# Optimization experiments

Hardware: AMD Instinct MI355X
Metric: run time of the kernel (lower is better)

## Reference

```python
import jax, jax.numpy as jnp
import numpy as np

B, S = 2, 2048          # 2 prompt sequences of 2048 tokens (packed: T = B*S)
H, KV, D, G = 32, 8, 128, 128   # heads, kv heads, head_dim, quant group size
THETA = 1e6


def _dequant(w_int, scales, g=G):
    # w_int: [O, I] int4 values in [-8, 7]; scales: [O, I//g] per-group fp scales
    return w_int.astype(jnp.float32) * jnp.repeat(scales, g, axis=1)


def _rope_neox(x, pos):
    # x: [B, S, h, D]; pos: [B, S]; neox style rotates (first half, second half)
    half = D // 2
    inv_freq = 1.0 / (THETA ** (jnp.arange(half, dtype=jnp.float32) / half))
    ang = pos[:, :, None] * inv_freq[None, None, :]          # [B, S, half]
    cos = jnp.cos(ang)[:, :, None, :]
    sin = jnp.sin(ang)[:, :, None, :]
    x1, x2 = x[..., :half], x[..., half:]
    return jnp.concatenate([x1 * cos - x2 * sin, x2 * cos + x1 * sin], axis=-1)


def setup_inputs() -> dict:
    key = jax.random.key(0)
    k1, k2, k3, k4, k5, k6 = jax.random.split(key, 6)
    T, HID = B * S, H * D
    q_hidden = jax.random.randint(k1, (T, HID), -127, 128, dtype=jnp.int32)  # int8 acts
    q_scale = jax.random.uniform(k2, (T,), dtype=jnp.float32) * 0.01 + 1e-4  # per-token scale
    q_sum = jnp.sum(q_hidden, axis=-1).astype(jnp.float32)                   # per-token int8 sum
    OUT_QKV = (H + 2 * KV) * D
    w_qkv = jax.random.randint(k3, (OUT_QKV, HID), -8, 8, dtype=jnp.int32)   # int4 weights
    s_qkv = jax.random.uniform(k4, (OUT_QKV, HID // G), dtype=jnp.float32) * 0.01 + 1e-4
    w_o = jax.random.randint(k5, (HID, HID), -8, 8, dtype=jnp.int32)
    s_o = jax.random.uniform(k6, (HID, HID // G), dtype=jnp.float32) * 0.01 + 1e-4
    return {"q_hidden": q_hidden, "q_scale": q_scale, "q_sum": q_sum,
            "w_qkv": w_qkv, "s_qkv": s_qkv, "w_o": w_o, "s_o": s_o}


def reference(q_hidden, q_scale, q_sum, w_qkv, s_qkv, w_o, s_o):
    T = q_hidden.shape[0]
    # W4A8 qkv_proj with dynamic per-token input scale (symmetric int4 -> sum unused)
    x = q_hidden.astype(jnp.float32) * q_scale[:, None]          # dequant activations
    qkv = x @ _dequant(w_qkv, s_qkv).T                            # [T, (H+2KV)*D]
    q_sz, kv_sz = H * D, KV * D
    q = qkv[:, :q_sz].reshape(B, S, H, D)
    k = qkv[:, q_sz:q_sz + kv_sz].reshape(B, S, KV, D)
    v = qkv[:, q_sz + kv_sz:].reshape(B, S, KV, D)
    # fused bias(none)+RoPE (neox, full head_dim)
    pos = jnp.broadcast_to(jnp.arange(S, dtype=jnp.float32), (B, S))
    q = _rope_neox(q, pos)
    k = _rope_neox(k, pos)
    # varlen causal flash attention (GQA: 4 q-heads per kv head)
    qg = q.reshape(B, S, KV, H // KV, D)
    scores = jnp.einsum('bsghd,btgd->bghst', qg, k) * (D ** -0.5)
    causal = jnp.tril(jnp.ones((S, S), dtype=bool))
    scores = jnp.where(causal[None, None, None], scores, -jnp.inf)
    p = jax.nn.softmax(scores, axis=-1)
    attn = jnp.einsum('bghst,btgd->bsghd', p, v).reshape(T, H * D)
    # invoke_quant_fuse_sum: per-token symmetric int8 requant of attn output
    amax = jnp.maximum(jnp.max(jnp.abs(attn), axis=-1, keepdims=True), 1e-6)
    a_scale = amax / 127.0
    attn_q = jnp.clip(jnp.round(attn / a_scale), -127.0, 127.0)
    # W4A8 o_proj
    out = (attn_q * a_scale) @ _dequant(w_o, s_o).T               # [T, H*D]
    return out
```

## Files before the change

kernel.cpp:

```cpp
#include <hip/hip_runtime.h>
#include <math.h>

#define B_ 2
#define S_ 2048
#define H_ 32
#define KV_ 8
#define D_ 128
#define T_ 4096
#define HID_ 4096
#define OQKV_ 6144

typedef __attribute__((ext_vector_type(4))) float f32x4;
typedef __attribute__((ext_vector_type(4))) int i32x4;
typedef __attribute__((ext_vector_type(8))) __bf16 bf16x8;
typedef __attribute__((ext_vector_type(8))) unsigned short u16x8;
typedef unsigned short u16;
typedef signed char s8;

__device__ __forceinline__ u16 f2b(float f) {
  unsigned x = __float_as_uint(f);
  return (u16)((x + 0x7FFFu + ((x >> 16) & 1u)) >> 16);
}
__device__ __forceinline__ float b2f(u16 u) {
  return __uint_as_float(((unsigned)u) << 16);
}

__device__ __forceinline__ void async16(const void* g, void* l) {
  __builtin_amdgcn_global_load_lds((__attribute__((address_space(1))) void*)g,
                                   (__attribute__((address_space(3))) void*)l,
                                   16, 0, 0);
}

__device__ __forceinline__ bf16x8 ld8(const u16* p) { return *(const bf16x8*)p; }

__device__ __forceinline__ f32x4 mfma16x16(bf16x8 a, bf16x8 b, f32x4 c) {
  return __builtin_amdgcn_mfma_f32_16x16x32_bf16(a, b, c, 0, 0, 0);
}

__device__ __forceinline__ bf16x8 ones8() {
  union { u16x8 u; bf16x8 b; } c;
  c.u = u16x8{0x3F80, 0x3F80, 0x3F80, 0x3F80, 0x3F80, 0x3F80, 0x3F80, 0x3F80};
  return c.b;
}

__global__ __launch_bounds__(256) void pack_i8(const int* __restrict__ w,
                                               s8* __restrict__ out) {
  size_t base = ((size_t)blockIdx.x * 256 + threadIdx.x) * 4;
  int4 v = *(const int4*)(w + base);
  unsigned r = (unsigned)(v.x & 255) | ((unsigned)(v.y & 255) << 8) |
               ((unsigned)(v.z & 255) << 16) | ((unsigned)v.w << 24);
  *(unsigned*)(out + base) = r;
}

__global__ __launch_bounds__(256) void rope_kernel(u16* __restrict__ qkv) {
  int idx = blockIdx.x * 256 + threadIdx.x;
  int t = idx / 2560;
  int r = idx - t * 2560;
  int head = r >> 6;
  int d = r & 63;
  int col = (head < 32) ? (head * 128 + d) : (4096 + (head - 32) * 128 + d);
  size_t base = (size_t)t * 6144 + col;
  float x1 = b2f(qkv[base]);
  float x2 = b2f(qkv[base + 64]);
  float e = (float)d * 0.015625f;
  float freq = exp2f(e * -19.931568569324174f);
  float ang = (float)(t & 2047) * freq;
  float sn, cs;
  sincosf(ang, &sn, &cs);
  qkv[base] = f2b(x1 * cs - x2 * sn);
  qkv[base + 64] = f2b(x2 * cs + x1 * sn);
}

__global__ __launch_bounds__(256) void vt_transpose(const u16* __restrict__ qkv,
                                                    u16* __restrict__ vt) {
  __shared__ u16 tile[64][65];
  const int s0 = blockIdx.x * 64, d0 = blockIdx.y * 64;
  const int bk = blockIdx.z, b = bk >> 3, kv = bk & 7;
  const int tid = threadIdx.x;
  const int rr = tid >> 3, cc = tid & 7;
#pragma unroll
  for (int it = 0; it < 2; it++) {
    int r = it * 32 + rr;
    u16x8 v = *(const u16x8*)(qkv + (size_t)(b * 2048 + s0 + r) * 6144 + 5120 +
                              kv * 128 + d0 + cc * 8);
#pragma unroll
    for (int k = 0; k < 8; k++) tile[r][cc * 8 + k] = v[k];
  }
  __syncthreads();
#pragma unroll
  for (int it = 0; it < 2; it++) {
    int d = it * 32 + rr;
    u16x8 o;
#pragma unroll
    for (int k = 0; k < 8; k++) o[k] = tile[cc * 8 + k][d];
    *(u16x8*)(vt + (size_t)(bk * 128 + d0 + d) * 2048 + s0 + cc * 8) = o;
  }
}

__device__ __forceinline__ void store_out(float* p, float v) { *p = v; }
__device__ __forceinline__ void store_out(u16* p, float v) { *p = f2b(v); }

template <typename OutT>
__global__ __launch_bounds__(256) void gemm_i8(const s8* __restrict__ A,
                                               const s8* __restrict__ Bw,
                                               const float* __restrict__ sB,
                                               const float* __restrict__ rowscale,
                                               OutT* __restrict__ C,
                                               int M, int N, int K) {
  __shared__ __align__(16) s8 As[128 * 64];
  __shared__ __align__(16) s8 Bs[128 * 64];
  __shared__ float Ss[128][33];
  const int tid = threadIdx.x;
  const int lane = tid & 63;
  const int wv = tid >> 6;
  const int wm = wv >> 1, wn = wv & 1;
  const int m0 = blockIdx.y * 128, n0 = blockIdx.x * 128;
  const int g = lane >> 4, c15 = lane & 15;
  const int KG = K >> 7;

  for (int i = tid; i < 128 * 32; i += 256)
    Ss[i >> 5][i & 31] = sB[(size_t)n0 * 32 + i];

  f32x4 acc[4][4] = {};

  const int c0 = 2 * wv, c1 = c0 + 1;
  const int srow = lane >> 2;
  const int pch = lane & 3;
  const int scol = (((pch - (srow >> 1)) & 3)) * 16;
  const s8* Ag0 = A + (size_t)(m0 + c0 * 16 + srow) * K + scol;
  const s8* Ag1 = A + (size_t)(m0 + c1 * 16 + srow) * K + scol;
  const s8* Bg0 = Bw + (size_t)(n0 + c0 * 16 + srow) * K + scol;
  const s8* Bg1 = Bw + (size_t)(n0 + c1 * 16 + srow) * K + scol;
  s8* Al0 = As + c0 * 1024 + lane * 16;
  s8* Al1 = As + c1 * 1024 + lane * 16;
  s8* Bl0 = Bs + c0 * 1024 + lane * 16;
  s8* Bl1 = Bs + c1 * 1024 + lane * 16;

  for (int grp = 0; grp < KG; grp++) {
    i32x4 iacc[4][4];
#pragma unroll
    for (int sub = 0; sub < 2; sub++) {
      const int kb = grp * 128 + sub * 64;
      __syncthreads();
      async16(Ag0 + kb, Al0);
      async16(Ag1 + kb, Al1);
      async16(Bg0 + kb, Bl0);
      async16(Bg1 + kb, Bl1);
      __syncthreads();
      i32x4 af[4], bf[4];
#pragma unroll
      for (int i = 0; i < 4; i++) {
        af[i] = *(const i32x4*)(As + (wm * 64 + i * 16 + c15) * 64 +
                                ((g + (c15 >> 1)) & 3) * 16);
        bf[i] = *(const i32x4*)(Bs + (wn * 64 + i * 16 + c15) * 64 +
                                ((g + (c15 >> 1)) & 3) * 16);
      }
#pragma unroll
      for (int i = 0; i < 4; i++)
#pragma unroll
        for (int j = 0; j < 4; j++)
          iacc[i][j] = __builtin_amdgcn_mfma_i32_16x16x64_i8(
              af[i], bf[j], sub ? iacc[i][j] : (i32x4){0, 0, 0, 0}, 0, 0, 0);
    }
#pragma unroll
    for (int j = 0; j < 4; j++) {
      const float sc = Ss[wn * 64 + j * 16 + c15][grp];
#pragma unroll
      for (int i = 0; i < 4; i++)
#pragma unroll
        for (int r = 0; r < 4; r++)
          acc[i][j][r] += sc * (float)iacc[i][j][r];
    }
  }

#pragma unroll
  for (int i = 0; i < 4; i++) {
#pragma unroll
    for (int r = 0; r < 4; r++) {
      int m = m0 + wm * 64 + i * 16 + g * 4 + r;
      float scm = rowscale[m];
#pragma unroll
      for (int j = 0; j < 4; j++) {
        int n = n0 + wn * 64 + j * 16 + c15;
        store_out(C + (size_t)m * N + n, acc[i][j][r] * scm);
      }
    }
  }
}

struct AttnState {
  f32x4 acc[2][9];
  float mrun[2][4];
};

template <bool FULL>
__device__ __forceinline__ void attn_step(
    int j0, int q0, const u16* kbase, const u16* vbase, u16* pw0, u16* pw1,
    const bf16x8 qf[2][4], AttnState& st, int g, int c15, const bf16x8 vones) {
  const int qmax = q0 + 31;
  f32x4 sc[2][4];
#pragma unroll
  for (int nt = 0; nt < 4; nt++) {
    if (FULL || (j0 + nt * 16 <= qmax)) {
      bf16x8 kf[4];
      const u16* kp = kbase + (size_t)(j0 + nt * 16) * 6144;
#pragma unroll
      for (int c = 0; c < 4; c++) kf[c] = ld8(kp + c * 32);
      f32x4 s0 = {0.f, 0.f, 0.f, 0.f}, s1 = {0.f, 0.f, 0.f, 0.f};
#pragma unroll
      for (int c = 0; c < 4; c++) {
        s0 = mfma16x16(qf[0][c], kf[c], s0);
        s1 = mfma16x16(qf[1][c], kf[c], s1);
      }
      if (FULL) {
#pragma unroll
        for (int r = 0; r < 4; r++) {
          sc[0][nt][r] = s0[r] * 0.08838834764831845f;
          sc[1][nt][r] = s1[r] * 0.08838834764831845f;
        }
      } else {
        const int key = j0 + nt * 16 + c15;
#pragma unroll
        for (int r = 0; r < 4; r++) {
          sc[0][nt][r] =
              (key <= q0 + g * 4 + r) ? s0[r] * 0.08838834764831845f : -INFINITY;
          sc[1][nt][r] =
              (key <= q0 + 16 + g * 4 + r) ? s1[r] * 0.08838834764831845f : -INFINITY;
        }
      }
    }
  }
#pragma unroll
  for (int m = 0; m < 2; m++) {
    u16* pw = m ? pw1 : pw0;
    float alpha[4];
#pragma unroll
    for (int r = 0; r < 4; r++) {
      float rm = -INFINITY;
#pragma unroll
      for (int nt = 0; nt < 4; nt++)
        if (FULL || (j0 + nt * 16 <= qmax)) rm = fmaxf(rm, sc[m][nt][r]);
      rm = fmaxf(rm, __shfl_xor(rm, 1));
      rm = fmaxf(rm, __shfl_xor(rm, 2));
      rm = fmaxf(rm, __shfl_xor(rm, 4));
      rm = fmaxf(rm, __shfl_xor(rm, 8));
      float mnew = fmaxf(st.mrun[m][r], rm);
      alpha[r] = __expf(st.mrun[m][r] - mnew);
      st.mrun[m][r] = mnew;
#pragma unroll
      for (int nt = 0; nt < 4; nt++) {
        float pv = (FULL || (j0 + nt * 16 <= qmax))
                       ? __expf(sc[m][nt][r] - mnew) : 0.0f;
        pw[(g * 4 + r) * 72 + nt * 16 + c15] = f2b(pv);
      }
    }
#pragma unroll
    for (int dt = 0; dt < 9; dt++)
#pragma unroll
      for (int r = 0; r < 4; r++) st.acc[m][dt][r] *= alpha[r];
  }
#pragma unroll
  for (int kc = 0; kc < 2; kc++) {
    bf16x8 pf0 = ld8(pw0 + c15 * 72 + kc * 32 + g * 8);
    bf16x8 pf1 = ld8(pw1 + c15 * 72 + kc * 32 + g * 8);
#pragma unroll
    for (int dt = 0; dt < 8; dt++) {
      bf16x8 vf = ld8(vbase + (size_t)(dt * 16) * 2048 + j0 + kc * 32);
      st.acc[0][dt] = mfma16x16(pf0, vf, st.acc[0][dt]);
      st.acc[1][dt] = mfma16x16(pf1, vf, st.acc[1][dt]);
    }
    st.acc[0][8] = mfma16x16(pf0, vones, st.acc[0][8]);
    st.acc[1][8] = mfma16x16(pf1, vones, st.acc[1][8]);
  }
}

__global__ __launch_bounds__(256, 2) void attn_kernel(const u16* __restrict__ qkvb,
                                                      const u16* __restrict__ vtb,
                                                      float* __restrict__ out) {
  __shared__ __align__(16) u16 Ps[4][2][16 * 72];
  const int tid = threadIdx.x, lane = tid & 63, wv = tid >> 6;
  const int g = lane >> 4, c15 = lane & 15;
  const int a = blockIdx.x * 4 + wv;
  const int h = blockIdx.y, b = blockIdx.z, kvh = h >> 2;
  const bf16x8 vones = ones8();
  const u16* kbase =
      qkvb + (size_t)(b * 2048 + c15) * 6144 + 4096 + kvh * 128 + g * 8;
  const u16* vbase = vtb + (size_t)((b * 8 + kvh) * 128 + c15) * 2048 + g * 8;
  u16* pw0 = &Ps[wv][0][0];
  u16* pw1 = &Ps[wv][1][0];

  for (int half = 0; half < 2; half++) {
    const int qt = half ? (63 - a) : a;
    const int q0 = qt * 32;
    bf16x8 qf[2][4];
#pragma unroll
    for (int m = 0; m < 2; m++) {
      const u16* qp =
          qkvb + (size_t)(b * 2048 + q0 + m * 16 + c15) * 6144 + h * 128 + g * 8;
#pragma unroll
      for (int c = 0; c < 4; c++) qf[m][c] = ld8(qp + c * 32);
    }
    AttnState st;
#pragma unroll
    for (int m = 0; m < 2; m++)
#pragma unroll
      for (int dt = 0; dt < 9; dt++) st.acc[m][dt] = f32x4{0.f, 0.f, 0.f, 0.f};
#pragma unroll
    for (int m = 0; m < 2; m++)
#pragma unroll
      for (int r = 0; r < 4; r++) st.mrun[m][r] = -INFINITY;

    const int nfull = qt >> 1;
    for (int jt = 0; jt < nfull; jt++)
      attn_step<true>(jt * 64, q0, kbase, vbase, pw0, pw1, qf, st, g, c15, vones);
    attn_step<false>(nfull * 64, q0, kbase, vbase, pw0, pw1, qf, st, g, c15, vones);

#pragma unroll
    for (int m = 0; m < 2; m++)
#pragma unroll
      for (int r = 0; r < 4; r++) {
        const int row = q0 + m * 16 + g * 4 + r;
        float inv = 1.0f / st.acc[m][8][r];
        float* op = out + (size_t)(b * 2048 + row) * 4096 + h * 128;
#pragma unroll
        for (int dt = 0; dt < 8; dt++) op[dt * 16 + c15] = st.acc[m][dt][r] * inv;
      }
  }
}

__global__ __launch_bounds__(256) void quant_kernel(const float* __restrict__ attn,
                                                    s8* __restrict__ aq,
                                                    float* __restrict__ ascale) {
  const int t = blockIdx.x, tid = threadIdx.x;
  const float* row = attn + (size_t)t * 4096;
  f32x4 v[4];
  float am = 0.f;
#pragma unroll
  for (int i = 0; i < 4; i++) {
    v[i] = *(const f32x4*)(row + tid * 16 + i * 4);
#pragma unroll
    for (int r = 0; r < 4; r++) am = fmaxf(am, fabsf(v[i][r]));
  }
#pragma unroll
  for (int m = 1; m <= 32; m <<= 1) am = fmaxf(am, __shfl_xor(am, m));
  __shared__ float red[4];
  if ((tid & 63) == 0) red[tid >> 6] = am;
  __syncthreads();
  am = fmaxf(fmaxf(red[0], red[1]), fmaxf(red[2], red[3]));
  float asc = fmaxf(am, 1e-6f) / 127.0f;
  if (tid == 0) ascale[t] = asc;
  int w[4];
#pragma unroll
  for (int i = 0; i < 4; i++) {
    int bytes[4];
#pragma unroll
    for (int r = 0; r < 4; r++) {
      float q = rintf(v[i][r] / asc);
      q = fminf(127.0f, fmaxf(-127.0f, q));
      bytes[r] = ((int)q) & 255;
    }
    w[i] = bytes[0] | (bytes[1] << 8) | (bytes[2] << 16) | (bytes[3] << 24);
  }
  *(int4*)(aq + (size_t)t * 4096 + tid * 16) = int4{w[0], w[1], w[2], w[3]};
}

extern "C" void kernel_launch(void* const* d_in, const int* in_sizes, int n_in,
                              void* d_out, int out_size, void* d_ws, size_t ws_size,
                              hipStream_t stream) {
  const int* q_hidden = (const int*)d_in[0];
  const float* q_scale = (const float*)d_in[1];
  const int* w_qkv = (const int*)d_in[3];
  const float* s_qkv = (const float*)d_in[4];
  const int* w_o = (const int*)d_in[5];
  const float* s_o = (const float*)d_in[6];
  float* out = (float*)d_out;

  char* ws = (char*)d_ws;
  const size_t MB = 1024 * 1024;
  s8* WB = (s8*)(ws);
  u16* QKVB = (u16*)(ws + 48 * MB);
  u16* VTB = (u16*)(ws);
  s8* ATTNQ = (s8*)(ws + 8 * MB);
  float* ASC = (float*)(ws + 25 * MB);
  s8* WOB = (s8*)(ws + 48 * MB);
  s8* XB = (s8*)d_out;

  pack_i8<<<16384, 256, 0, stream>>>(q_hidden, XB);
  pack_i8<<<24576, 256, 0, stream>>>(w_qkv, WB);
  gemm_i8<u16><<<dim3(48, 32), 256, 0, stream>>>(XB, WB, s_qkv, q_scale, QKVB,
                                                 T_, OQKV_, HID_);
  rope_kernel<<<40960, 256, 0, stream>>>(QKVB);
  vt_transpose<<<dim3(32, 2, 16), 256, 0, stream>>>(QKVB, VTB);
  attn_kernel<<<dim3(8, 32, 2), 256, 0, stream>>>(QKVB, VTB, out);
  quant_kernel<<<4096, 256, 0, stream>>>(out, ATTNQ, ASC);
  pack_i8<<<16384, 256, 0, stream>>>(w_o, WOB);
  gemm_i8<float><<<dim3(32, 32), 256, 0, stream>>>(ATTNQ, WOB, s_o, ASC, out,
                                                   T_, HID_, HID_);
}
```

Baseline: 802.4 us.

## Split attention KV loop across wave pairs with shared-memory softmax merge

Each query tile is now handled by two waves, each covering half of the causal KV range. The partial accumulators and running maxima are merged through shared memory with a rescaled flash-decoding style combine. The grid doubles and launch bounds request 4 blocks per CU, aiming for more parallelism and occupancy in the attention kernel. The cost is extra block-wide syncs, shared-memory traffic, and possible register pressure or spills under the tighter launch bound.

Result: slower. 997.3 us (+24.3%).

```diff
diff --git a/kernel.cpp b/kernel.cpp
--- a/kernel.cpp
+++ b/kernel.cpp
@@ -274,13 +274,15 @@
   }
 }
 
-__global__ __launch_bounds__(256, 2) void attn_kernel(const u16* __restrict__ qkvb,
+__global__ __launch_bounds__(256, 4) void attn_kernel(const u16* __restrict__ qkvb,
                                                       const u16* __restrict__ vtb,
                                                       float* __restrict__ out) {
   __shared__ __align__(16) u16 Ps[4][2][16 * 72];
+  __shared__ __align__(16) float Sc[2][10][64][4];
   const int tid = threadIdx.x, lane = tid & 63, wv = tid >> 6;
   const int g = lane >> 4, c15 = lane & 15;
-  const int a = blockIdx.x * 4 + wv;
+  const int pair = wv & 1, sub = wv >> 1;
+  const int a = blockIdx.x * 2 + pair;
   const int h = blockIdx.y, b = blockIdx.z, kvh = h >> 2;
   const bf16x8 vones = ones8();
   const u16* kbase =
@@ -311,20 +313,59 @@
       for (int r = 0; r < 4; r++) st.mrun[m][r] = -INFINITY;
 
     const int nfull = qt >> 1;
-    for (int jt = 0; jt < nfull; jt++)
-      attn_step<true>(jt * 64, q0, kbase, vbase, pw0, pw1, qf, st, g, c15, vones);
-    attn_step<false>(nfull * 64, q0, kbase, vbase, pw0, pw1, qf, st, g, c15, vones);
-
-#pragma unroll
-    for (int m = 0; m < 2; m++)
-#pragma unroll
-      for (int r = 0; r < 4; r++) {
-        const int row = q0 + m * 16 + g * 4 + r;
-        float inv = 1.0f / st.acc[m][8][r];
-        float* op = out + (size_t)(b * 2048 + row) * 4096 + h * 128;
-#pragma unroll
-        for (int dt = 0; dt < 8; dt++) op[dt * 16 + c15] = st.acc[m][dt][r] * inv;
-      }
+    const int ns = nfull + 1;
+    const int ns0 = ns >> 1;
+    if (sub == 0) {
+      for (int jt = 0; jt < ns0; jt++)
+        attn_step<true>(jt * 64, q0, kbase, vbase, pw0, pw1, qf, st, g, c15, vones);
+    } else {
+      for (int jt = ns0; jt < nfull; jt++)
+        attn_step<true>(jt * 64, q0, kbase, vbase, pw0, pw1, qf, st, g, c15, vones);
+      attn_step<false>(nfull * 64, q0, kbase, vbase, pw0, pw1, qf, st, g, c15, vones);
+    }
+
+#pragma unroll
+    for (int mt = 0; mt < 2; mt++) {
+      __syncthreads();
+      if (sub == 1) {
+#pragma unroll
+        for (int dt = 0; dt < 9; dt++)
+          *(f32x4*)&Sc[pair][dt][lane][0] = st.acc[mt][dt];
+        *(f32x4*)&Sc[pair][9][lane][0] =
+            f32x4{st.mrun[mt][0], st.mrun[mt][1], st.mrun[mt][2], st.mrun[mt][3]};
+      }
+      __syncthreads();
+      if (sub == 0) {
+        f32x4 m2 = *(const f32x4*)&Sc[pair][9][lane][0];
+        float a0[4], a1[4];
+#pragma unroll
+        for (int r = 0; r < 4; r++) {
+          float mn = fmaxf(st.mrun[mt][r], m2[r]);
+          a0[r] = __expf(st.mrun[mt][r] - mn);
+          a1[r] = __expf(m2[r] - mn);
+        }
+#pragma unroll
+        for (int dt = 0; dt < 9; dt++) {
+          f32x4 o = *(const f32x4*)&Sc[pair][dt][lane][0];
+#pragma unroll
+          for (int r = 0; r < 4; r++)
+            st.acc[mt][dt][r] = st.acc[mt][dt][r] * a0[r] + o[r] * a1[r];
+        }
+      }
+    }
+
+    if (sub == 0) {
+#pragma unroll
+      for (int m = 0; m < 2; m++)
+#pragma unroll
+        for (int r = 0; r < 4; r++) {
+          const int row = q0 + m * 16 + g * 4 + r;
+          float inv = 1.0f / st.acc[m][8][r];
+          float* op = out + (size_t)(b * 2048 + row) * 4096 + h * 128;
+#pragma unroll
+          for (int dt = 0; dt < 8; dt++) op[dt * 16 + c15] = st.acc[m][dt][r] * inv;
+        }
+    }
   }
 }
 
@@ -391,7 +432,7 @@
                                                  T_, OQKV_, HID_);
   rope_kernel<<<40960, 256, 0, stream>>>(QKVB);
   vt_transpose<<<dim3(32, 2, 16), 256, 0, stream>>>(QKVB, VTB);
-  attn_kernel<<<dim3(8, 32, 2), 256, 0, stream>>>(QKVB, VTB, out);
+  attn_kernel<<<dim3(16, 32, 2), 256, 0, stream>>>(QKVB, VTB, out);
   quant_kernel<<<4096, 256, 0, stream>>>(out, ATTNQ, ASC);
   pack_i8<<<16384, 256, 0, stream>>>(w_o, WOB);
   gemm_i8<float><<<dim3(32, 32), 256, 0, stream>>>(ATTNQ, WOB, s_o, ASC, out,
```

## Stage K/V tiles in shared memory with async double-buffered loads in attention

Applied to the files above, without the earlier changes.

The attention kernel now assigns each block a 128-row query tile (four warps of 32 rows) and cooperatively stages 64-key K and V tiles into swizzled shared memory with async copies. V is double-buffered so the next tile loads during softmax and PV. This replaces per-warp direct global loads and removes redundant K/V traffic across the warps of a block. The grid is reordered to launch the heaviest causal tiles first. The price is extra LDS use, two barriers per step, and the loss of the earlier pairing of short and long tiles inside each warp for load balance.

Result: faster. 693.9 us (-13.5%).

```diff
diff --git a/kernel.cpp b/kernel.cpp
--- a/kernel.cpp
+++ b/kernel.cpp
@@ -188,24 +188,25 @@
   }
 }
 
+
 struct AttnState {
   f32x4 acc[2][9];
   float mrun[2][4];
 };
 
 template <bool FULL>
-__device__ __forceinline__ void attn_step(
-    int j0, int q0, const u16* kbase, const u16* vbase, u16* pw0, u16* pw1,
-    const bf16x8 qf[2][4], AttnState& st, int g, int c15, const bf16x8 vones) {
-  const int qmax = q0 + 31;
-  f32x4 sc[2][4];
+__device__ __forceinline__ void qk_phase(int j0, int q0w, const u16* Ksp,
+                                         const bf16x8 qf[2][4],
+                                         f32x4 (&sc)[2][4], int g, int c15) {
+  const int qmax = q0w + 31;
 #pragma unroll
   for (int nt = 0; nt < 4; nt++) {
     if (FULL || (j0 + nt * 16 <= qmax)) {
       bf16x8 kf[4];
-      const u16* kp = kbase + (size_t)(j0 + nt * 16) * 6144;
-#pragma unroll
-      for (int c = 0; c < 4; c++) kf[c] = ld8(kp + c * 32);
+#pragma unroll
+      for (int c = 0; c < 4; c++)
+        kf[c] = ld8(Ksp + (nt * 16 + c15) * 128 +
+                    (((g + 4 * c) ^ (c15 & 7)) * 8));
       f32x4 s0 = {0.f, 0.f, 0.f, 0.f}, s1 = {0.f, 0.f, 0.f, 0.f};
 #pragma unroll
       for (int c = 0; c < 4; c++) {
@@ -223,13 +224,21 @@
 #pragma unroll
         for (int r = 0; r < 4; r++) {
           sc[0][nt][r] =
-              (key <= q0 + g * 4 + r) ? s0[r] * 0.08838834764831845f : -INFINITY;
+              (key <= q0w + g * 4 + r) ? s0[r] * 0.08838834764831845f : -INFINITY;
           sc[1][nt][r] =
-              (key <= q0 + 16 + g * 4 + r) ? s1[r] * 0.08838834764831845f : -INFINITY;
+              (key <= q0w + 16 + g * 4 + r) ? s1[r] * 0.08838834764831845f : -INFINITY;
         }
       }
     }
   }
+}
+
+template <bool FULL>
+__device__ __forceinline__ void smax_pv(int j0, int q0w, const u16* Vsp,
+                                        u16* pw0, u16* pw1, f32x4 (&sc)[2][4],
+                                        AttnState& st, int g, int c15,
+                                        const bf16x8 vones) {
+  const int qmax = q0w + 31;
 #pragma unroll
   for (int m = 0; m < 2; m++) {
     u16* pw = m ? pw1 : pw0;
@@ -265,7 +274,8 @@
     bf16x8 pf1 = ld8(pw1 + c15 * 72 + kc * 32 + g * 8);
 #pragma unroll
     for (int dt = 0; dt < 8; dt++) {
-      bf16x8 vf = ld8(vbase + (size_t)(dt * 16) * 2048 + j0 + kc * 32);
+      bf16x8 vf = ld8(Vsp + (dt * 16 + c15) * 64 +
+                      (((g + 4 * kc) ^ (c15 & 7)) * 8));
       st.acc[0][dt] = mfma16x16(pf0, vf, st.acc[0][dt]);
       st.acc[1][dt] = mfma16x16(pf1, vf, st.acc[1][dt]);
     }
@@ -277,55 +287,90 @@
 __global__ __launch_bounds__(256, 2) void attn_kernel(const u16* __restrict__ qkvb,
                                                       const u16* __restrict__ vtb,
                                                       float* __restrict__ out) {
+  __shared__ __align__(16) u16 Ks[64 * 128];
+  __shared__ __align__(16) u16 Vs[2][128 * 64];
   __shared__ __align__(16) u16 Ps[4][2][16 * 72];
   const int tid = threadIdx.x, lane = tid & 63, wv = tid >> 6;
   const int g = lane >> 4, c15 = lane & 15;
-  const int a = blockIdx.x * 4 + wv;
-  const int h = blockIdx.y, b = blockIdx.z, kvh = h >> 2;
+  const int h = blockIdx.x, b = blockIdx.y, qb = 15 - (int)blockIdx.z;
+  const int kvh = h >> 2;
+  const int Q0 = qb * 128;
+  const int q0w = Q0 + wv * 32;
+  const int nsteps = 2 * qb + 2;
   const bf16x8 vones = ones8();
-  const u16* kbase =
-      qkvb + (size_t)(b * 2048 + c15) * 6144 + 4096 + kvh * 128 + g * 8;
-  const u16* vbase = vtb + (size_t)((b * 8 + kvh) * 128 + c15) * 2048 + g * 8;
   u16* pw0 = &Ps[wv][0][0];
   u16* pw1 = &Ps[wv][1][0];
 
-  for (int half = 0; half < 2; half++) {
-    const int qt = half ? (63 - a) : a;
-    const int q0 = qt * 32;
-    bf16x8 qf[2][4];
-#pragma unroll
-    for (int m = 0; m < 2; m++) {
-      const u16* qp =
-          qkvb + (size_t)(b * 2048 + q0 + m * 16 + c15) * 6144 + h * 128 + g * 8;
-#pragma unroll
-      for (int c = 0; c < 4; c++) qf[m][c] = ld8(qp + c * 32);
-    }
-    AttnState st;
-#pragma unroll
-    for (int m = 0; m < 2; m++)
-#pragma unroll
-      for (int dt = 0; dt < 9; dt++) st.acc[m][dt] = f32x4{0.f, 0.f, 0.f, 0.f};
-#pragma unroll
-    for (int m = 0; m < 2; m++)
-#pragma unroll
-      for (int r = 0; r < 4; r++) st.mrun[m][r] = -INFINITY;
-
-    const int nfull = qt >> 1;
-    for (int jt = 0; jt < nfull; jt++)
-      attn_step<true>(jt * 64, q0, kbase, vbase, pw0, pw1, qf, st, g, c15, vones);
-    attn_step<false>(nfull * 64, q0, kbase, vbase, pw0, pw1, qf, st, g, c15, vones);
-
-#pragma unroll
-    for (int m = 0; m < 2; m++)
-#pragma unroll
-      for (int r = 0; r < 4; r++) {
-        const int row = q0 + m * 16 + g * 4 + r;
-        float inv = 1.0f / st.acc[m][8][r];
-        float* op = out + (size_t)(b * 2048 + row) * 4096 + h * 128;
-#pragma unroll
-        for (int dt = 0; dt < 8; dt++) op[dt * 16 + c15] = st.acc[m][dt][r] * inv;
-      }
-  }
+  const int keyl = lane >> 4, kch = lane & 15;
+  const int dll = lane >> 3, vch = lane & 7;
+  const u16* Kg = qkvb + (size_t)(b * 2048) * 6144 + 4096 + kvh * 128;
+  const u16* Vg = vtb + (size_t)((b * 8 + kvh) * 128) * 2048;
+
+  auto stageK = [&](int j0) {
+#pragma unroll
+    for (int i = 0; i < 4; i++) {
+      const int key = wv * 16 + i * 4 + keyl;
+      async16(Kg + (size_t)(j0 + key) * 6144 + ((kch ^ (key & 7)) * 8),
+              (u16*)Ks + (wv * 16 + i * 4) * 128 + lane * 8);
+    }
+  };
+  auto stageV = [&](int j0, int vb) {
+#pragma unroll
+    for (int i = 0; i < 4; i++) {
+      const int d = wv * 32 + i * 8 + dll;
+      async16(Vg + (size_t)d * 2048 + j0 + ((vch ^ (d & 7)) * 8),
+              (u16*)&Vs[vb][0] + (wv * 32 + i * 8) * 64 + lane * 8);
+    }
+  };
+
+  bf16x8 qf[2][4];
+#pragma unroll
+  for (int m = 0; m < 2; m++) {
+    const u16* qp =
+        qkvb + (size_t)(b * 2048 + q0w + m * 16 + c15) * 6144 + h * 128 + g * 8;
+#pragma unroll
+    for (int c = 0; c < 4; c++) qf[m][c] = ld8(qp + c * 32);
+  }
+
+  AttnState st;
+#pragma unroll
+  for (int m = 0; m < 2; m++) {
+#pragma unroll
+    for (int dt = 0; dt < 9; dt++) st.acc[m][dt] = f32x4{0.f, 0.f, 0.f, 0.f};
+#pragma unroll
+    for (int r = 0; r < 4; r++) st.mrun[m][r] = -INFINITY;
+  }
+
+  stageK(0);
+  stageV(0, 0);
+
+  for (int jt = 0; jt < nsteps; ++jt) {
+    const int j0 = jt * 64;
+    __syncthreads();
+    const int mode = (j0 + 64 <= q0w) ? 0 : ((j0 <= q0w + 31) ? 1 : 2);
+    f32x4 sc[2][4];
+    if (mode == 0) qk_phase<true>(j0, q0w, (const u16*)Ks, qf, sc, g, c15);
+    else if (mode == 1) qk_phase<false>(j0, q0w, (const u16*)Ks, qf, sc, g, c15);
+    __syncthreads();
+    if (jt + 1 < nsteps) {
+      stageK(j0 + 64);
+      stageV(j0 + 64, (jt + 1) & 1);
+    }
+    const u16* Vsp = (const u16*)&Vs[jt & 1][0];
+    if (mode == 0) smax_pv<true>(j0, q0w, Vsp, pw0, pw1, sc, st, g, c15, vones);
+    else if (mode == 1) smax_pv<false>(j0, q0w, Vsp, pw0, pw1, sc, st, g, c15, vones);
+  }
+
+#pragma unroll
+  for (int m = 0; m < 2; m++)
+#pragma unroll
+    for (int r = 0; r < 4; r++) {
+      const int row = q0w + m * 16 + g * 4 + r;
+      float inv = 1.0f / st.acc[m][8][r];
+      float* op = out + (size_t)(b * 2048 + row) * 4096 + h * 128;
+#pragma unroll
+      for (int dt = 0; dt < 8; dt++) op[dt * 16 + c15] = st.acc[m][dt][r] * inv;
+    }
 }
 
 __global__ __launch_bounds__(256) void quant_kernel(const float* __restrict__ attn,
@@ -391,7 +436,7 @@
                                                  T_, OQKV_, HID_);
   rope_kernel<<<40960, 256, 0, stream>>>(QKVB);
   vt_transpose<<<dim3(32, 2, 16), 256, 0, stream>>>(QKVB, VTB);
-  attn_kernel<<<dim3(8, 32, 2), 256, 0, stream>>>(QKVB, VTB, out);
+  attn_kernel<<<dim3(32, 2, 16), 256, 0, stream>>>(QKVB, VTB, out);
   quant_kernel<<<4096, 256, 0, stream>>>(out, ATTNQ, ASC);
   pack_i8<<<16384, 256, 0, stream>>>(w_o, WOB);
   gemm_i8<float><<<dim3(32, 32), 256, 0, stream>>>(ATTNQ, WOB, s_o, ASC, out,
```
